# Optimization experiments

Hardware: AMD Instinct MI355X
Metric: run time of the kernel (lower is better)

Reference implementation:

```python
import jax, jax.numpy as jnp
import numpy as np

BATCH = 8
TABLE_NUM = 16          # levels L
TABLE_DIM = 8192        # entries per table
RES_MIN, RES_MAX = 16, 256
SAMPLE_RES = 256
N = SAMPLE_RES * SAMPLE_RES
CH = TABLE_NUM * 2      # feature dim per level is 2
STYLE_DIM = 512
PRIME = np.uint32(2654435761)
LN_EPS = 1e-5
DEMOD_EPS = 1e-8

# geometric level resolutions (Instant-NGP style)
_b = np.exp((np.log(RES_MAX) - np.log(RES_MIN)) / (TABLE_NUM - 1))
RES_LIST = [int(np.floor(RES_MIN * (_b ** l))) for l in range(TABLE_NUM)]


def _corner_idx_weights(coords):
    """coords [N,2] in [0,1] -> (idx [L,N,4] int32 flat into L*T, w [L,N,4])."""
    idx_all, w_all = [], []
    for l, res in enumerate(RES_LIST):
        pos = coords * (res - 1)                     # [N,2]
        p0f = jnp.floor(pos)
        frac = pos - p0f                              # bilinear fractions
        p0 = jnp.clip(p0f.astype(jnp.int32), 0, res - 2)
        x0, y0 = p0[:, 0], p0[:, 1]
        x1, y1 = x0 + 1, y0 + 1
        fx, fy = frac[:, 0], frac[:, 1]
        cx = jnp.stack([x0, x1, x0, x1], -1)          # [N,4]
        cy = jnp.stack([y0, y0, y1, y1], -1)
        w = jnp.stack([(1 - fx) * (1 - fy), fx * (1 - fy),
                       (1 - fx) * fy, fx * fy], -1)   # [N,4]
        if res * res <= TABLE_DIM:                    # dense grid fits: direct index
            idx = cy * res + cx
        else:                                         # spatial hash
            h = cx.astype(jnp.uint32) ^ (cy.astype(jnp.uint32) * PRIME)
            idx = (h % jnp.uint32(TABLE_DIM)).astype(jnp.int32)
        idx_all.append(idx + l * TABLE_DIM)
        w_all.append(w)
    return jnp.stack(idx_all), jnp.stack(w_all)       # [L,N,4]


def _hash_retrieve(tables, idx, w):
    """tables [B,L,T,2] -> bilinear multi-res lookup [B,N,2L]."""
    B = tables.shape[0]
    tf = tables.reshape(B, TABLE_NUM * TABLE_DIM, 2)
    g = tf[:, idx.reshape(-1)]                        # [B, L*N*4, 2]
    g = g.reshape(B, TABLE_NUM, N, 4, 2)
    feats = jnp.einsum('blncf,lnc->blnf', g, w)       # [B,L,N,2]
    return feats.transpose(0, 2, 1, 3).reshape(B, N, CH)


def _hash_recon(tokens, idx, w):
    """tokens [B,N,2L] -> transpose scatter back into tables [B,L,T,2]."""
    B = tokens.shape[0]
    t = tokens.reshape(B, N, TABLE_NUM, 2).transpose(0, 2, 1, 3)   # [B,L,N,2]
    contrib = jnp.einsum('blnf,lnc->blncf', t, w)                   # [B,L,N,4,2]
    out = jnp.zeros((B, TABLE_NUM * TABLE_DIM, 2), tokens.dtype)
    out = out.at[:, idx.reshape(-1)].add(contrib.reshape(B, -1, 2))
    return out.reshape(B, TABLE_NUM, TABLE_DIM, 2)


def _synthesis_layer(x, s, affine_w, affine_b, conv_w, conv_b):
    """StyleGAN2 modulated 3x3 conv (demodulate, up=1) + bias + lrelu*sqrt(2)."""
    styles = s @ (affine_w.T / np.sqrt(STYLE_DIM)) + affine_b       # [B,ch]
    xm = x * styles[:, :, None, None]                               # modulate input
    y = jax.lax.conv_general_dilated(xm, conv_w, (1, 1), [(1, 1), (1, 1)],
                                     dimension_numbers=('NCHW', 'OIHW', 'NCHW'))
    # demod coef: rsqrt(sum_{i,k,l} (w_oikl * style_i)^2 + eps)
    dcoef = jax.lax.rsqrt(jnp.einsum('oikl,bi->bo', conv_w * conv_w,
                                     styles * styles) + DEMOD_EPS)
    y = y * dcoef[:, :, None, None] + conv_b[None, :, None, None]
    return jax.nn.leaky_relu(y, 0.2) * np.sqrt(2.0)


def setup_inputs() -> dict:
    key = jax.random.key(0)
    k1, k2, k3, k4 = jax.random.split(key, 4)
    inputs = jax.random.normal(k1, (BATCH, TABLE_NUM, 2 * TABLE_DIM), jnp.float32)
    s = jax.random.normal(k2, (BATCH, STYLE_DIM), jnp.float32)
    g = jnp.linspace(0.0, 1.0, SAMPLE_RES)
    yy, xx = jnp.meshgrid(g, g, indexing='ij')
    coords = jnp.stack([xx, yy], -1).reshape(N, 2).astype(jnp.float32)
    affine_w = jax.random.normal(k3, (CH, STYLE_DIM), jnp.float32)
    affine_b = jnp.ones((CH,), jnp.float32)          # bias_init=1
    conv_w = jax.random.normal(k4, (CH, CH, 3, 3), jnp.float32)
    conv_b = jnp.zeros((CH,), jnp.float32)
    return {"inputs": inputs, "s": s, "coords": coords,
            "affine_w": affine_w, "affine_b": affine_b,
            "conv_w": conv_w, "conv_b": conv_b}


def reference(inputs, s, coords, affine_w, affine_b, conv_w, conv_b):
    B = inputs.shape[0]
    tables = inputs.reshape(B, TABLE_NUM, TABLE_DIM, 2)
    idx, w = _corner_idx_weights(coords)
    feats = _hash_retrieve(tables, idx, w)                 # [B,N,ch]
    block = feats.reshape(B, SAMPLE_RES, SAMPLE_RES, CH).transpose(0, 3, 1, 2)
    block = _synthesis_layer(block, s, affine_w, affine_b, conv_w, conv_b)
    tokens = block.reshape(B, CH, N).transpose(0, 2, 1)    # [B,N,ch]
    recon = _hash_recon(tokens, idx, w)                    # [B,L,T,2]
    out = recon.reshape(B, TABLE_NUM, -1) + inputs         # residual
    mu = out.mean(-1, keepdims=True)
    var = ((out - mu) ** 2).mean(-1, keepdims=True)
    return (out - mu) * jax.lax.rsqrt(var + LN_EPS)        # layer_norm, no affine
```

## Files before the change

kernel.cpp:

```cpp
#include <hip/hip_runtime.h>
#include <hip/hip_fp16.h>
#include <cmath>
#include <cstdint>

#define NB 8
#define NL 16
#define TD 8192
#define NPIX 65536
#define CH 32
#define SD 512

static constexpr uint32_t PRIME = 2654435761u;

typedef __attribute__((ext_vector_type(8))) _Float16 f16x8;
typedef __attribute__((ext_vector_type(4))) float f32x4;

static constexpr int cNCX[16] = {4,5,5,5,6,6,7,7,8,9,10,12,13,15,18,20};
static constexpr int CTOFF[17] = {0,16,41,66,91,127,163,212,261,325,406,506,650,819,1044,1368,1768};

struct LevelParams {
    int res[NL];
    int hashed[NL];
    int uoff[NL];
    int soff[NL];
    int cwoff[NL];
    int nck[NL];
    int sumr;
    int nwaves;
};

__device__ __forceinline__ unsigned short f2bf(float f) {
    uint32_t u = __float_as_uint(f);
    return (unsigned short)((u + 0x7fffu + ((u >> 16) & 1u)) >> 16);
}
__device__ __forceinline__ float bflo(uint32_t u) { return __uint_as_float(u << 16); }
__device__ __forceinline__ float bfhi(uint32_t u) { return __uint_as_float(u & 0xffff0000u); }
__device__ __forceinline__ uint32_t packbf(float a, float b) {
    return (uint32_t)f2bf(a) | ((uint32_t)f2bf(b) << 16);
}
__device__ __forceinline__ uint32_t packh2(float a, float b) {
    return (uint32_t)__half_as_ushort(__float2half_rn(a)) |
           ((uint32_t)__half_as_ushort(__float2half_rn(b)) << 16);
}
__device__ __forceinline__ float h2lo(uint32_t u) {
    return __half2float(__ushort_as_half((unsigned short)(u & 0xffffu)));
}
__device__ __forceinline__ float h2hi(uint32_t u) {
    return __half2float(__ushort_as_half((unsigned short)(u >> 16)));
}
__device__ __forceinline__ __half2 u2h2(uint32_t u) {
    union { uint32_t u; __half2 h; } v; v.u = u; return v.h;
}
__device__ __forceinline__ uint32_t h22u(__half2 h) {
    union { __half2 h; uint32_t u; } v; v.h = h; return v.u;
}

__global__ __launch_bounds__(256) void k_prep(
    const float* __restrict__ s, const float* __restrict__ aw,
    const float* __restrict__ ab, const float* __restrict__ cw,
    const float* __restrict__ coords,
    float* __restrict__ styles, float* __restrict__ dcoef,
    int* __restrict__ ctab, float* __restrict__ ftab, int* __restrict__ stab,
    unsigned short* __restrict__ wpack, float* __restrict__ R, LevelParams p) {
    int bb = blockIdx.x;
    int t = threadIdx.x;
    if (bb < NB) {
        int b = bb;
        int c = t >> 3, part = t & 7;
        const float* sv = s + b * SD + part * 64;
        const float* wv = aw + c * SD + part * 64;
        float acc = 0.f;
        #pragma unroll 8
        for (int k = 0; k < 64; ++k) acc += sv[k] * wv[k];
        acc += __shfl_xor(acc, 1, 64);
        acc += __shfl_xor(acc, 2, 64);
        acc += __shfl_xor(acc, 4, 64);
        __shared__ float st_sh[CH];
        if (part == 0) {
            float st = acc * 0.04419417382415922f  + ab[c];
            styles[b * CH + c] = st;
            st_sh[c] = st;
        }
        __syncthreads();
        if (t < CH) {
            float d = 0.f;
            for (int i = 0; i < CH; ++i) {
                const float* w9 = cw + (t * CH + i) * 9;
                float ws = 0.f;
                #pragma unroll
                for (int k = 0; k < 9; ++k) ws += w9[k] * w9[k];
                float si = st_sh[i];
                d += ws * si * si;
            }
            dcoef[b * CH + t] = rsqrtf(d + 1e-8f);
        }
    } else if (bb < NB + NL) {
        int l = bb - NB;
        int j = t;
        int r = p.res[l];
        float g = coords[2 * j];
        float px = g * (float)(r - 1);
        float fl = floorf(px);
        float f = px - fl;
        int c = min((int)fl, r - 2);
        ctab[l * 256 + j] = c;
        ftab[l * 256 + j] = f;
        __shared__ int cs[256];
        cs[j] = c;
        __syncthreads();
        for (int cc = j; cc <= r; cc += 256) {
            int cnt = 0;
            for (int i = 0; i < 256; ++i) cnt += (cs[i] < cc) ? 1 : 0;
            stab[p.soff[l] + cc] = cnt;
        }
    } else if (bb < NB + NL + 36) {
        int idx = (bb - NB - NL) * 256 + t;
        if (idx < 9 * 4 * 32 * 8) {
            int j = idx & 7;
            int o = (idx >> 3) & 31;
            int kgi = (idx >> 8) & 3;
            int tap = idx >> 10;
            wpack[idx] = __half_as_ushort(__float2half_rn(cw[(o * 32 + kgi * 8 + j) * 9 + tap]));
        }
    } else {
        float4* Rv = (float4*)R;
        int base = (bb - NB - NL - 36) * 1024;
        float4 z = make_float4(0.f, 0.f, 0.f, 0.f);
        #pragma unroll
        for (int q = 0; q < 4; ++q)
            Rv[base + q * 256 + t] = z;
    }
}

__global__ __launch_bounds__(256) void k_gather(
    const float* __restrict__ tables, const int* __restrict__ ctab,
    const float* __restrict__ styles, uint32_t* __restrict__ ctileG,
    LevelParams p) {
    __shared__ int cxbase[NL], cybase[NL], ncxA[NL], ncyA[NL];
    int bid = blockIdx.x;
    int b = bid & 7;
    int t = bid >> 3;
    int tx0 = (t & 15) * 16, ty0 = (t >> 4) * 16;
    int tid = threadIdx.x;
    const float* tb = tables + (size_t)b * NL * TD * 2;
    if (tid < NL) {
        int l = tid;
        int cxb = ctab[l * 256 + max(tx0 - 1, 0)];
        int cyb = ctab[l * 256 + max(ty0 - 1, 0)];
        cxbase[l] = cxb;
        cybase[l] = cyb;
        ncxA[l] = ctab[l * 256 + min(tx0 + 16, 255)] - cxb + 2;
        ncyA[l] = ctab[l * 256 + min(ty0 + 16, 255)] - cyb + 2;
    }
    __syncthreads();
    uint32_t* out = ctileG + (size_t)bid * 1768;
    #pragma unroll
    for (int l = 0; l < NL; ++l) {
        const int NCXl = cNCX[l];
        const int CAP = (CTOFF[l + 1] - CTOFF[l]);
        float s0 = styles[b * CH + 2 * l], s1 = styles[b * CH + 2 * l + 1];
        for (int u2 = tid; u2 < CAP; u2 += 256) {
            int sy = u2 / NCXl;
            int sx = u2 - sy * NCXl;
            uint32_t val = 0u;
            if (sx < ncxA[l] && sy < ncyA[l]) {
                int ax = cxbase[l] + sx, ay = cybase[l] + sy;
                int r = p.res[l];
                uint32_t idx = p.hashed[l]
                    ? (((uint32_t)ax ^ ((uint32_t)ay * PRIME)) & (TD - 1))
                    : (uint32_t)(ay * r + ax);
                float2 g = *(const float2*)(tb + (size_t)l * TD * 2 + 2 * idx);
                val = packh2(g.x * s0, g.y * s1);
            }
            out[CTOFF[l] + u2] = val;
        }
    }
}

template<int L>
__device__ __forceinline__ uint32_t feat1p(const uint4& cp, const uint4& rp,
                                           const uint32_t* ctile) {
    int a = CTOFF[L] + (int)rp.x * cNCX[L] + (int)cp.x;
    __half2 c00 = u2h2(ctile[a]), c10 = u2h2(ctile[a + 1]);
    __half2 c01 = u2h2(ctile[a + cNCX[L]]), c11 = u2h2(ctile[a + cNCX[L] + 1]);
    __half2 wxA = u2h2(cp.y), wxB = u2h2(cp.z);
    __half2 t0 = __hfma2(wxB, c10, __hmul2(wxA, c00));
    __half2 t1 = __hfma2(wxB, c11, __hmul2(wxA, c01));
    __half2 f = __hfma2(u2h2(rp.z), t1, __hmul2(u2h2(rp.y), t0));
    return h22u(f);
}

template<int L0>
__device__ __forceinline__ void phase1(int lane, int tx0, int ty0,
                                       const uint4* colP, const uint4* rowP,
                                       const uint32_t* ctile, uint32_t* xt) {
    constexpr int q = L0 / 4;
    #pragma unroll
    for (int it = 0; it < 6; ++it) {
        int pl = it * 64 + lane;
        int rr = pl / 18, cc = pl - rr * 18;
        int gy = ty0 + rr - 1, gx = tx0 + cc - 1;
        uint4 v = make_uint4(0u, 0u, 0u, 0u);
        if (pl < 324 && (unsigned)gy < 256u && (unsigned)gx < 256u) {
            uint4 cp0 = colP[(L0 + 0) * 18 + cc], rp0 = rowP[(L0 + 0) * 18 + rr];
            uint4 cp1 = colP[(L0 + 1) * 18 + cc], rp1 = rowP[(L0 + 1) * 18 + rr];
            uint4 cp2 = colP[(L0 + 2) * 18 + cc], rp2 = rowP[(L0 + 2) * 18 + rr];
            uint4 cp3 = colP[(L0 + 3) * 18 + cc], rp3 = rowP[(L0 + 3) * 18 + rr];
            v.x = feat1p<L0 + 0>(cp0, rp0, ctile);
            v.y = feat1p<L0 + 1>(cp1, rp1, ctile);
            v.z = feat1p<L0 + 2>(cp2, rp2, ctile);
            v.w = feat1p<L0 + 3>(cp3, rp3, ctile);
        }
        if (pl < 324)
            *(uint4*)(xt + (size_t)(pl * 4 + (q ^ (cc & 3))) * 4) = v;
    }
}

__global__ __launch_bounds__(256) void k_conv(
    const uint32_t* __restrict__ ctileG, const int* __restrict__ ctab,
    const float* __restrict__ ftab,
    const unsigned short* __restrict__ wpack, const float* __restrict__ cb,
    const float* __restrict__ dcoef, uint32_t* __restrict__ tokens,
    LevelParams p) {
    __shared__ uint32_t xt[18 * 18 * 16];
    __shared__ uint32_t ctile[1768];
    __shared__ uint4 colP[NL * 18];
    __shared__ uint4 rowP[NL * 18];
    __shared__ int cxbase[NL], cybase[NL];

    int bid = blockIdx.x;
    int b = bid & 7;
    int t = bid >> 3;
    int tx0 = (t & 15) * 16, ty0 = (t >> 4) * 16;
    int tid = threadIdx.x;
    int lane = tid & 63, wv = tid >> 6;
    int npx = lane & 15, kg = lane >> 4;

    if (tid < NL) {
        int l = tid;
        cxbase[l] = ctab[l * 256 + max(tx0 - 1, 0)];
        cybase[l] = ctab[l * 256 + max(ty0 - 1, 0)];
    }
    {
        const uint4* src = (const uint4*)(ctileG + (size_t)bid * 1768);
        for (int i = tid; i < 442; i += 256)
            *(uint4*)(ctile + i * 4) = src[i];
    }
    __syncthreads();
    for (int u0 = tid; u0 < NL * 36; u0 += 256) {
        int l = u0 / 36, pos = u0 - l * 36;
        if (pos < 18) {
            int gx = tx0 - 1 + pos;
            int gxc = min(max(gx, 0), 255);
            float f = ftab[l * 256 + gxc];
            colP[l * 18 + pos] = make_uint4(
                (uint32_t)(ctab[l * 256 + gxc] - cxbase[l]),
                h22u(__float2half2_rn(1.f - f)), h22u(__float2half2_rn(f)), 0u);
        } else {
            int pr = pos - 18;
            int gy = ty0 - 1 + pr;
            int gyc = min(max(gy, 0), 255);
            float f = ftab[l * 256 + gyc];
            rowP[l * 18 + pr] = make_uint4(
                (uint32_t)(ctab[l * 256 + gyc] - cybase[l]),
                h22u(__float2half2_rn(1.f - f)), h22u(__float2half2_rn(f)), 0u);
        }
    }
    __syncthreads();

    switch (wv) {
        case 0: phase1<0>(lane, tx0, ty0, colP, rowP, ctile, xt); break;
        case 1: phase1<4>(lane, tx0, ty0, colP, rowP, ctile, xt); break;
        case 2: phase1<8>(lane, tx0, ty0, colP, rowP, ctile, xt); break;
        default: phase1<12>(lane, tx0, ty0, colP, rowP, ctile, xt); break;
    }
    __builtin_amdgcn_sched_barrier(0);

    f16x8 wf[9][2];
    #pragma unroll
    for (int tp = 0; tp < 9; ++tp) {
        wf[tp][0] = *(const f16x8*)(wpack + (size_t)((tp * 4 + kg) * 32 + npx) * 8);
        wf[tp][1] = *(const f16x8*)(wpack + (size_t)((tp * 4 + kg) * 32 + 16 + npx) * 8);
    }
    float dc[2][4], bs[2][4];
    #pragma unroll
    for (int ob = 0; ob < 2; ++ob)
        #pragma unroll
        for (int rg = 0; rg < 4; ++rg) {
            int oc = ob * 16 + kg * 4 + rg;
            dc[ob][rg] = dcoef[b * CH + oc];
            bs[ob][rg] = cb[oc];
        }
    __syncthreads();

    #pragma unroll 1
    for (int it = 0; it < 4; ++it) {
        int py_l = it * 4 + wv;
        int px_l = npx;
        f32x4 a0 = {0.f, 0.f, 0.f, 0.f};
        f32x4 a1 = {0.f, 0.f, 0.f, 0.f};
        #pragma unroll
        for (int ky = 0; ky < 3; ++ky) {
            int rowb = (py_l + ky) * 18;
            #pragma unroll
            for (int kx = 0; kx < 3; ++kx) {
                int cc = px_l + kx;
                f16x8 bf = *(const f16x8*)(xt + (((rowb + cc) << 2) + (kg ^ (cc & 3))) * 4);
                a0 = __builtin_amdgcn_mfma_f32_16x16x32_f16(wf[ky * 3 + kx][0], bf, a0, 0, 0, 0);
                a1 = __builtin_amdgcn_mfma_f32_16x16x32_f16(wf[ky * 3 + kx][1], bf, a1, 0, 0, 0);
            }
        }
        int py = ty0 + py_l, px = tx0 + px_l;
        size_t pbase = (size_t)py * 256 + px;
        {
            float y0 = a0[0] * dc[0][0] + bs[0][0];
            float y1 = a0[1] * dc[0][1] + bs[0][1];
            float y2 = a0[2] * dc[0][2] + bs[0][2];
            float y3 = a0[3] * dc[0][3] + bs[0][3];
            y0 = (y0 > 0.f ? y0 : 0.2f * y0) * 1.4142135623730951f;
            y1 = (y1 > 0.f ? y1 : 0.2f * y1) * 1.4142135623730951f;
            y2 = (y2 > 0.f ? y2 : 0.2f * y2) * 1.4142135623730951f;
            y3 = (y3 > 0.f ? y3 : 0.2f * y3) * 1.4142135623730951f;
            int lp0 = kg * 2;
            tokens[((size_t)(b * NL + lp0)) * NPIX + pbase] = packbf(y0, y1);
            tokens[((size_t)(b * NL + lp0 + 1)) * NPIX + pbase] = packbf(y2, y3);
        }
        {
            float y0 = a1[0] * dc[1][0] + bs[1][0];
            float y1 = a1[1] * dc[1][1] + bs[1][1];
            float y2 = a1[2] * dc[1][2] + bs[1][2];
            float y3 = a1[3] * dc[1][3] + bs[1][3];
            y0 = (y0 > 0.f ? y0 : 0.2f * y0) * 1.4142135623730951f;
            y1 = (y1 > 0.f ? y1 : 0.2f * y1) * 1.4142135623730951f;
            y2 = (y2 > 0.f ? y2 : 0.2f * y2) * 1.4142135623730951f;
            y3 = (y3 > 0.f ? y3 : 0.2f * y3) * 1.4142135623730951f;
            int lp0 = 8 + kg * 2;
            tokens[((size_t)(b * NL + lp0)) * NPIX + pbase] = packbf(y0, y1);
            tokens[((size_t)(b * NL + lp0 + 1)) * NPIX + pbase] = packbf(y2, y3);
        }
    }
}

__global__ __launch_bounds__(256) void k_recon1(const uint32_t* __restrict__ tokens,
                                                const int* __restrict__ ctab,
                                                const float* __restrict__ ftab,
                                                const int* __restrict__ stab,
                                                uint32_t* __restrict__ U, LevelParams p) {
    __shared__ float2 cf[256];
    __shared__ int sl[260];
    __shared__ uint32_t tok[8][256];
    int bid = blockIdx.x;
    int b = bid & 7;
    int rest = bid >> 3;
    int l = rest >> 5;
    int grp = rest & 31;
    int tid = threadIdx.x;
    int lane = tid & 63, wv = tid >> 6;
    int r = p.res[l];

    cf[tid] = make_float2(__int_as_float(ctab[l * 256 + tid]), ftab[l * 256 + tid]);
    for (int q = tid; q <= r; q += 256) sl[q] = stab[p.soff[l] + q];
    int i0 = grp * 8 + wv * 2;
    const uint32_t* trow = tokens + (size_t)(b * NL + l) * NPIX + i0 * 256;
    *(uint4*)&tok[wv * 2 + 0][lane * 4] = *(const uint4*)(trow + lane * 4);
    *(uint4*)&tok[wv * 2 + 1][lane * 4] = *(const uint4*)(trow + 256 + lane * 4);
    __syncthreads();

    uint32_t* Ul0 = U + (size_t)b * (p.sumr * 256) + p.uoff[l] + (size_t)i0 * r;
    uint32_t* Ul1 = Ul0 + r;
    int nck = p.nck[l];
    #pragma unroll 1
    for (int ck = 0; ck < nck; ++ck) {
        int cx = ck * 64 + lane;
        bool valid = cx < r;
        int jlo = 0, jhi = -1;
        if (valid) {
            jlo = (cx > 0) ? sl[cx - 1] : 0;
            jhi = sl[min(cx + 1, r)] - 1;
        }
        float a00 = 0.f, a01 = 0.f, a10 = 0.f, a11 = 0.f;
        for (int j = jlo; j <= jhi; ++j) {
            float2 cfv = cf[j];
            int c = __float_as_int(cfv.x);
            float f = cfv.y;
            float w = (c == cx) ? (1.f - f) : f;
            uint32_t tv0 = tok[wv * 2 + 0][j];
            uint32_t tv1 = tok[wv * 2 + 1][j];
            a00 += w * bflo(tv0);
            a01 += w * bfhi(tv0);
            a10 += w * bflo(tv1);
            a11 += w * bfhi(tv1);
        }
        if (valid) {
            Ul0[cx] = packh2(a00, a01);
            Ul1[cx] = packh2(a10, a11);
        }
    }
}

__global__ __launch_bounds__(256) void k_recon2(const uint32_t* __restrict__ U,
                                                const int* __restrict__ ctab,
                                                const float* __restrict__ ftab,
                                                const int* __restrict__ stab,
                                                float* __restrict__ R, LevelParams p) {
    int bid = blockIdx.x;
    int b = bid & 7;
    int bx = bid >> 3;
    int wid = bx * 4 + (threadIdx.x >> 6);
    int lane = threadIdx.x & 63;
    if (wid >= p.nwaves) return;
    int l = 0;
    #pragma unroll
    for (int q = 1; q < NL; ++q) if (wid >= p.cwoff[q]) l = q;
    int u = wid - p.cwoff[l];
    int r = p.res[l];
    int nck = p.nck[l];
    int cy = u / nck;
    int ck = u - cy * nck;
    int cx = ck * 64 + lane;
    bool valid = cx < r;
    const int* Sl = stab + p.soff[l];
    int ilo = (cy > 0) ? Sl[cy - 1] : 0;
    int ihi = Sl[min(cy + 1, r)] - 1;
    const uint32_t* Ub = U + (size_t)b * (p.sumr * 256) + p.uoff[l];
    const int* crow = ctab + l * 256;
    const float* frow = ftab + l * 256;
    float a0 = 0.f, a1 = 0.f;
    for (int i = ilo; i <= ihi; ++i) {
        int c = crow[i];
        float f = frow[i];
        float w = (c == cy) ? (1.f - f) : f;
        if (valid) {
            uint32_t uu = Ub[(size_t)i * r + cx];
            a0 += w * h2lo(uu);
            a1 += w * h2hi(uu);
        }
    }
    if (!valid) return;
    float* Rbl = R + (size_t)(b * NL + l) * TD * 2;
    if (p.hashed[l]) {
        uint32_t h = ((uint32_t)cx ^ ((uint32_t)cy * PRIME)) & (TD - 1);
        atomicAdd(&Rbl[2 * h], a0);
        atomicAdd(&Rbl[2 * h + 1], a1);
    } else {
        *(float2*)(Rbl + 2 * (cy * r + cx)) = make_float2(a0, a1);
    }
}

__global__ __launch_bounds__(512) void k_ln(const float* __restrict__ R,
                                            const float* __restrict__ inp,
                                            float* __restrict__ out) {
    int bid = blockIdx.x;
    int row = (bid & 7) * NL + (bid >> 3);
    const float4* rv = (const float4*)(R + (size_t)row * 16384);
    const float4* iv = (const float4*)(inp + (size_t)row * 16384);
    int tid = threadIdx.x;
    float sum = 0.f, ssq = 0.f;
    for (int k = tid; k < 4096; k += 512) {
        float4 a = rv[k], c = iv[k];
        float x0 = a.x + c.x, x1 = a.y + c.y, x2 = a.z + c.z, x3 = a.w + c.w;
        sum += x0 + x1 + x2 + x3;
        ssq += x0 * x0 + x1 * x1 + x2 * x2 + x3 * x3;
    }
    #pragma unroll
    for (int off = 32; off > 0; off >>= 1) {
        sum += __shfl_xor(sum, off, 64);
        ssq += __shfl_xor(ssq, off, 64);
    }
    __shared__ float red[16];
    int w = tid >> 6;
    if ((tid & 63) == 0) { red[w * 2] = sum; red[w * 2 + 1] = ssq; }
    __syncthreads();
    sum = 0.f; ssq = 0.f;
    #pragma unroll
    for (int q = 0; q < 8; ++q) { sum += red[q * 2]; ssq += red[q * 2 + 1]; }
    float mu = sum * (1.f / 16384.f);
    float var = ssq * (1.f / 16384.f) - mu * mu;
    float inv = rsqrtf(var + 1e-5f);
    float4* ob = (float4*)(out + (size_t)row * 16384);
    for (int k = tid; k < 4096; k += 512) {
        float4 a = rv[k], c = iv[k];
        float4 o4;
        o4.x = (a.x + c.x - mu) * inv;
        o4.y = (a.y + c.y - mu) * inv;
        o4.z = (a.z + c.z - mu) * inv;
        o4.w = (a.w + c.w - mu) * inv;
        ob[k] = o4;
    }
}

extern "C" void kernel_launch(void* const* d_in, const int* in_sizes, int n_in,
                              void* d_out, int out_size, void* d_ws, size_t ws_size,
                              hipStream_t stream) {
    const float* inputs = (const float*)d_in[0];
    const float* s      = (const float*)d_in[1];
    const float* coords = (const float*)d_in[2];
    const float* aw     = (const float*)d_in[3];
    const float* ab     = (const float*)d_in[4];
    const float* cw     = (const float*)d_in[5];
    const float* cb     = (const float*)d_in[6];

    char* ws = (char*)d_ws;
    uint32_t* U      = (uint32_t*)(ws);
    uint32_t* ctileG = (uint32_t*)(ws + 16777216);
    uint32_t* tokens = (uint32_t*)(ws + 33554432);
    float*    R      = (float*)(ws + 67108864);
    float*    styles = (float*)(ws + 75497472);
    float*    dcoef  = (float*)(ws + 75498496);
    int*      ctab   = (int*)(ws + 75499520);
    float*    ftab   = (float*)(ws + 75515904);
    int*      stab   = (int*)(ws + 75532288);
    unsigned short* wpack = (unsigned short*)(ws + 75540480);

    LevelParams p;
    double bb = exp((log(256.0) - log(16.0)) / 15.0);
    int uoff = 0, soff = 0, cwoff = 0, sumr = 0;
    for (int l = 0; l < NL; ++l) {
        int r = (int)floor(16.0 * pow(bb, (double)l));
        p.res[l] = r;
        p.hashed[l] = (r * r > TD) ? 1 : 0;
        p.uoff[l] = uoff;
        p.soff[l] = soff;
        p.cwoff[l] = cwoff;
        int nck = (r + 63) >> 6;
        p.nck[l] = nck;
        uoff += r * 256;
        soff += r + 2;
        cwoff += r * nck;
        sumr += r;
    }
    p.sumr = sumr;
    p.nwaves = cwoff;

    hipLaunchKernelGGL(k_prep, dim3(NB + NL + 36 + 512), dim3(256), 0, stream,
                       s, aw, ab, cw, coords, styles, dcoef, ctab, ftab, stab, wpack, R, p);
    hipLaunchKernelGGL(k_gather, dim3(2048), dim3(256), 0, stream,
                       inputs, ctab, styles, ctileG, p);
    hipLaunchKernelGGL(k_conv, dim3(2048), dim3(256), 0, stream,
                       ctileG, ctab, ftab, wpack, cb, dcoef, tokens, p);
    hipLaunchKernelGGL(k_recon1, dim3(NL * 32 * NB), dim3(256), 0, stream,
                       tokens, ctab, ftab, stab, U, p);
    hipLaunchKernelGGL(k_recon2, dim3(((p.nwaves + 3) / 4) * NB), dim3(256), 0, stream,
                       U, ctab, ftab, stab, R, p);
    hipLaunchKernelGGL(k_ln, dim3(NB * NL), dim3(512), 0, stream,
                       R, inputs, (float*)d_out);
}
```

Baseline: 98.67 us.

## Move bilinear feature interpolation into gather kernel, store full feature map

The gather stage now also computes the bilinear-interpolated fp16 features for each 16x16 tile and writes a full per-pixel feature map to global memory. The conv kernel then only loads an 18x18 halo of precomputed features into shared memory before the MFMA loop. This removes the redundant halo interpolation and the corner-tile reload from the conv kernel. In exchange it writes and reads a larger intermediate (64 bytes per pixel), and the halo pixels are read from neighbouring tiles' output.

```diff
diff --git a/kernel.cpp b/kernel.cpp
--- a/kernel.cpp
+++ b/kernel.cpp
@@ -132,51 +132,6 @@
     }
 }
 
-__global__ __launch_bounds__(256) void k_gather(
-    const float* __restrict__ tables, const int* __restrict__ ctab,
-    const float* __restrict__ styles, uint32_t* __restrict__ ctileG,
-    LevelParams p) {
-    __shared__ int cxbase[NL], cybase[NL], ncxA[NL], ncyA[NL];
-    int bid = blockIdx.x;
-    int b = bid & 7;
-    int t = bid >> 3;
-    int tx0 = (t & 15) * 16, ty0 = (t >> 4) * 16;
-    int tid = threadIdx.x;
-    const float* tb = tables + (size_t)b * NL * TD * 2;
-    if (tid < NL) {
-        int l = tid;
-        int cxb = ctab[l * 256 + max(tx0 - 1, 0)];
-        int cyb = ctab[l * 256 + max(ty0 - 1, 0)];
-        cxbase[l] = cxb;
-        cybase[l] = cyb;
-        ncxA[l] = ctab[l * 256 + min(tx0 + 16, 255)] - cxb + 2;
-        ncyA[l] = ctab[l * 256 + min(ty0 + 16, 255)] - cyb + 2;
-    }
-    __syncthreads();
-    uint32_t* out = ctileG + (size_t)bid * 1768;
-    #pragma unroll
-    for (int l = 0; l < NL; ++l) {
-        const int NCXl = cNCX[l];
-        const int CAP = (CTOFF[l + 1] - CTOFF[l]);
-        float s0 = styles[b * CH + 2 * l], s1 = styles[b * CH + 2 * l + 1];
-        for (int u2 = tid; u2 < CAP; u2 += 256) {
-            int sy = u2 / NCXl;
-            int sx = u2 - sy * NCXl;
-            uint32_t val = 0u;
-            if (sx < ncxA[l] && sy < ncyA[l]) {
-                int ax = cxbase[l] + sx, ay = cybase[l] + sy;
-                int r = p.res[l];
-                uint32_t idx = p.hashed[l]
-                    ? (((uint32_t)ax ^ ((uint32_t)ay * PRIME)) & (TD - 1))
-                    : (uint32_t)(ay * r + ax);
-                float2 g = *(const float2*)(tb + (size_t)l * TD * 2 + 2 * idx);
-                val = packh2(g.x * s0, g.y * s1);
-            }
-            out[CTOFF[l] + u2] = val;
-        }
-    }
-}
-
 template<int L>
 __device__ __forceinline__ uint32_t feat1p(const uint4& cp, const uint4& rp,
                                            const uint32_t* ctile) {
@@ -191,42 +146,109 @@
 }
 
 template<int L0>
-__device__ __forceinline__ void phase1(int lane, int tx0, int ty0,
-                                       const uint4* colP, const uint4* rowP,
-                                       const uint32_t* ctile, uint32_t* xt) {
+__device__ __forceinline__ void feat_body(int lane, int tx0, int ty0,
+                                          const uint4* colP, const uint4* rowP,
+                                          const uint32_t* ctile,
+                                          uint32_t* __restrict__ fb) {
     constexpr int q = L0 / 4;
     #pragma unroll
-    for (int it = 0; it < 6; ++it) {
+    for (int it = 0; it < 4; ++it) {
         int pl = it * 64 + lane;
-        int rr = pl / 18, cc = pl - rr * 18;
-        int gy = ty0 + rr - 1, gx = tx0 + cc - 1;
-        uint4 v = make_uint4(0u, 0u, 0u, 0u);
-        if (pl < 324 && (unsigned)gy < 256u && (unsigned)gx < 256u) {
-            uint4 cp0 = colP[(L0 + 0) * 18 + cc], rp0 = rowP[(L0 + 0) * 18 + rr];
-            uint4 cp1 = colP[(L0 + 1) * 18 + cc], rp1 = rowP[(L0 + 1) * 18 + rr];
-            uint4 cp2 = colP[(L0 + 2) * 18 + cc], rp2 = rowP[(L0 + 2) * 18 + rr];
-            uint4 cp3 = colP[(L0 + 3) * 18 + cc], rp3 = rowP[(L0 + 3) * 18 + rr];
-            v.x = feat1p<L0 + 0>(cp0, rp0, ctile);
-            v.y = feat1p<L0 + 1>(cp1, rp1, ctile);
-            v.z = feat1p<L0 + 2>(cp2, rp2, ctile);
-            v.w = feat1p<L0 + 3>(cp3, rp3, ctile);
-        }
-        if (pl < 324)
-            *(uint4*)(xt + (size_t)(pl * 4 + (q ^ (cc & 3))) * 4) = v;
-    }
-}
-
-__global__ __launch_bounds__(256) void k_conv(
-    const uint32_t* __restrict__ ctileG, const int* __restrict__ ctab,
-    const float* __restrict__ ftab,
+        int py_l = pl >> 4, px_l = pl & 15;
+        uint4 cp0 = colP[(L0 + 0) * 16 + px_l], rp0 = rowP[(L0 + 0) * 16 + py_l];
+        uint4 cp1 = colP[(L0 + 1) * 16 + px_l], rp1 = rowP[(L0 + 1) * 16 + py_l];
+        uint4 cp2 = colP[(L0 + 2) * 16 + px_l], rp2 = rowP[(L0 + 2) * 16 + py_l];
+        uint4 cp3 = colP[(L0 + 3) * 16 + px_l], rp3 = rowP[(L0 + 3) * 16 + py_l];
+        uint4 v;
+        v.x = feat1p<L0 + 0>(cp0, rp0, ctile);
+        v.y = feat1p<L0 + 1>(cp1, rp1, ctile);
+        v.z = feat1p<L0 + 2>(cp2, rp2, ctile);
+        v.w = feat1p<L0 + 3>(cp3, rp3, ctile);
+        size_t px = (size_t)(ty0 + py_l) * 256 + (tx0 + px_l);
+        *(uint4*)(fb + px * 16 + q * 4) = v;
+    }
+}
+
+__global__ __launch_bounds__(256) void k_feat(
+    const float* __restrict__ tables, const int* __restrict__ ctab,
+    const float* __restrict__ ftab, const float* __restrict__ styles,
+    uint32_t* __restrict__ featG, LevelParams p) {
+    __shared__ uint32_t ctile[1768];
+    __shared__ uint4 colP[NL * 16];
+    __shared__ uint4 rowP[NL * 16];
+    __shared__ int cxbase[NL], cybase[NL], ncxA[NL], ncyA[NL];
+
+    int bid = blockIdx.x;
+    int b = bid & 7;
+    int t = bid >> 3;
+    int tx0 = (t & 15) * 16, ty0 = (t >> 4) * 16;
+    int tid = threadIdx.x;
+    int lane = tid & 63, wv = tid >> 6;
+    const float* tb = tables + (size_t)b * NL * TD * 2;
+
+    if (tid < NL) {
+        int l = tid;
+        int cxb = ctab[l * 256 + max(tx0 - 1, 0)];
+        int cyb = ctab[l * 256 + max(ty0 - 1, 0)];
+        cxbase[l] = cxb;
+        cybase[l] = cyb;
+        ncxA[l] = ctab[l * 256 + min(tx0 + 16, 255)] - cxb + 2;
+        ncyA[l] = ctab[l * 256 + min(ty0 + 16, 255)] - cyb + 2;
+    }
+    __syncthreads();
+    for (int u0 = tid; u0 < NL * 32; u0 += 256) {
+        int l = u0 >> 5, pos = u0 & 31;
+        if (pos < 16) {
+            int gx = tx0 + pos;
+            float f = ftab[l * 256 + gx];
+            colP[l * 16 + pos] = make_uint4(
+                (uint32_t)(ctab[l * 256 + gx] - cxbase[l]),
+                h22u(__float2half2_rn(1.f - f)), h22u(__float2half2_rn(f)), 0u);
+        } else {
+            int pr = pos - 16;
+            int gy = ty0 + pr;
+            float f = ftab[l * 256 + gy];
+            rowP[l * 16 + pr] = make_uint4(
+                (uint32_t)(ctab[l * 256 + gy] - cybase[l]),
+                h22u(__float2half2_rn(1.f - f)), h22u(__float2half2_rn(f)), 0u);
+        }
+    }
+    #pragma unroll
+    for (int l = 0; l < NL; ++l) {
+        const int NCXl = cNCX[l];
+        const int CAP = (CTOFF[l + 1] - CTOFF[l]);
+        float s0 = styles[b * CH + 2 * l], s1 = styles[b * CH + 2 * l + 1];
+        for (int u2 = tid; u2 < CAP; u2 += 256) {
+            int sy = u2 / NCXl;
+            int sx = u2 - sy * NCXl;
+            if (sx < ncxA[l] && sy < ncyA[l]) {
+                int ax = cxbase[l] + sx, ay = cybase[l] + sy;
+                int r = p.res[l];
+                uint32_t idx = p.hashed[l]
+                    ? (((uint32_t)ax ^ ((uint32_t)ay * PRIME)) & (TD - 1))
+                    : (uint32_t)(ay * r + ax);
+                float2 g = *(const float2*)(tb + (size_t)l * TD * 2 + 2 * idx);
+                ctile[CTOFF[l] + sy * NCXl + sx] = packh2(g.x * s0, g.y * s1);
+            }
+        }
+    }
+    __syncthreads();
+
+    uint32_t* fb = featG + ((size_t)b << 16) * 16;
+    switch (wv) {
+        case 0: feat_body<0>(lane, tx0, ty0, colP, rowP, ctile, fb); break;
+        case 1: feat_body<4>(lane, tx0, ty0, colP, rowP, ctile, fb); break;
+        case 2: feat_body<8>(lane, tx0, ty0, colP, rowP, ctile, fb); break;
+        default: feat_body<12>(lane, tx0, ty0, colP, rowP, ctile, fb); break;
+    }
+}
+
+__global__ __launch_bounds__(256) void k_mfma(
+    const uint32_t* __restrict__ featG,
     const unsigned short* __restrict__ wpack, const float* __restrict__ cb,
     const float* __restrict__ dcoef, uint32_t* __restrict__ tokens,
     LevelParams p) {
     __shared__ uint32_t xt[18 * 18 * 16];
-    __shared__ uint32_t ctile[1768];
-    __shared__ uint4 colP[NL * 18];
-    __shared__ uint4 rowP[NL * 18];
-    __shared__ int cxbase[NL], cybase[NL];
 
     int bid = blockIdx.x;
     int b = bid & 7;
@@ -235,46 +257,7 @@
     int tid = threadIdx.x;
     int lane = tid & 63, wv = tid >> 6;
     int npx = lane & 15, kg = lane >> 4;
-
-    if (tid < NL) {
-        int l = tid;
-        cxbase[l] = ctab[l * 256 + max(tx0 - 1, 0)];
-        cybase[l] = ctab[l * 256 + max(ty0 - 1, 0)];
-    }
-    {
-        const uint4* src = (const uint4*)(ctileG + (size_t)bid * 1768);
-        for (int i = tid; i < 442; i += 256)
-            *(uint4*)(ctile + i * 4) = src[i];
-    }
-    __syncthreads();
-    for (int u0 = tid; u0 < NL * 36; u0 += 256) {
-        int l = u0 / 36, pos = u0 - l * 36;
-        if (pos < 18) {
-            int gx = tx0 - 1 + pos;
-            int gxc = min(max(gx, 0), 255);
-            float f = ftab[l * 256 + gxc];
-            colP[l * 18 + pos] = make_uint4(
-                (uint32_t)(ctab[l * 256 + gxc] - cxbase[l]),
-                h22u(__float2half2_rn(1.f - f)), h22u(__float2half2_rn(f)), 0u);
-        } else {
-            int pr = pos - 18;
-            int gy = ty0 - 1 + pr;
-            int gyc = min(max(gy, 0), 255);
-            float f = ftab[l * 256 + gyc];
-            rowP[l * 18 + pr] = make_uint4(
-                (uint32_t)(ctab[l * 256 + gyc] - cybase[l]),
-                h22u(__float2half2_rn(1.f - f)), h22u(__float2half2_rn(f)), 0u);
-        }
-    }
-    __syncthreads();
-
-    switch (wv) {
-        case 0: phase1<0>(lane, tx0, ty0, colP, rowP, ctile, xt); break;
-        case 1: phase1<4>(lane, tx0, ty0, colP, rowP, ctile, xt); break;
-        case 2: phase1<8>(lane, tx0, ty0, colP, rowP, ctile, xt); break;
-        default: phase1<12>(lane, tx0, ty0, colP, rowP, ctile, xt); break;
-    }
-    __builtin_amdgcn_sched_barrier(0);
+    const uint32_t* fb = featG + ((size_t)b << 16) * 16;
 
     f16x8 wf[9][2];
     #pragma unroll
@@ -291,6 +274,16 @@
             dc[ob][rg] = dcoef[b * CH + oc];
             bs[ob][rg] = cb[oc];
         }
+
+    for (int idx = tid; idx < 18 * 18 * 4; idx += 256) {
+        int pl = idx >> 2, q = idx & 3;
+        int rr = pl / 18, cc = pl - rr * 18;
+        int gy = ty0 + rr - 1, gx = tx0 + cc - 1;
+        uint4 v = make_uint4(0u, 0u, 0u, 0u);
+        if ((unsigned)gy < 256u && (unsigned)gx < 256u)
+            v = *(const uint4*)(fb + ((size_t)gy * 256 + gx) * 16 + q * 4);
+        *(uint4*)(xt + (size_t)(pl * 4 + (q ^ (cc & 3))) * 4) = v;
+    }
     __syncthreads();
 
     #pragma unroll 1
@@ -501,8 +494,8 @@
     const float* cb     = (const float*)d_in[6];
 
     char* ws = (char*)d_ws;
+    uint32_t* featG  = (uint32_t*)(ws);
     uint32_t* U      = (uint32_t*)(ws);
-    uint32_t* ctileG = (uint32_t*)(ws + 16777216);
     uint32_t* tokens = (uint32_t*)(ws + 33554432);
     float*    R      = (float*)(ws + 67108864);
     float*    styles = (float*)(ws + 75497472);
@@ -534,10 +527,10 @@
 
     hipLaunchKernelGGL(k_prep, dim3(NB + NL + 36 + 512), dim3(256), 0, stream,
                        s, aw, ab, cw, coords, styles, dcoef, ctab, ftab, stab, wpack, R, p);
-    hipLaunchKernelGGL(k_gather, dim3(2048), dim3(256), 0, stream,
-                       inputs, ctab, styles, ctileG, p);
-    hipLaunchKernelGGL(k_conv, dim3(2048), dim3(256), 0, stream,
-                       ctileG, ctab, ftab, wpack, cb, dcoef, tokens, p);
+    hipLaunchKernelGGL(k_feat, dim3(2048), dim3(256), 0, stream,
+                       inputs, ctab, ftab, styles, featG, p);
+    hipLaunchKernelGGL(k_mfma, dim3(2048), dim3(256), 0, stream,
+                       featG, wpack, cb, dcoef, tokens, p);
     hipLaunchKernelGGL(k_recon1, dim3(NL * 32 * NB), dim3(256), 0, stream,
                        tokens, ctab, ftab, stab, U, p);
     hipLaunchKernelGGL(k_recon2, dim3(((p.nwaves + 3) / 4) * NB), dim3(256), 0, stream,
```

New measurement: 103.1 us. 1.05x slower.
